# Kernel optimization log

Hardware: AMD Instinct MI355X
Metric: run time of the kernel (lower is better)

Reference implementation:

```python
import jax, jax.numpy as jnp
import numpy as np

N_NODES = 100000

def setup_inputs() -> dict:
    key = jax.random.key(0)
    k1, k2, k3, k4, k5 = jax.random.split(key, 5)
    node_emb = jax.random.normal(k1, (100000, 128), dtype=jnp.float32)
    edge_weight = jax.random.uniform(k2, (1600000,), dtype=jnp.float32)
    src = jax.random.randint(k3, (1600000,), 0, 100000, dtype=jnp.int32)
    dst = jax.random.randint(k4, (1600000,), 0, 100000, dtype=jnp.int32)
    W = jax.random.normal(k5, (128, 128), dtype=jnp.float32) * (1.0 / np.sqrt(128))
    return {"node_emb": node_emb, "edge_weight": edge_weight, "src": src, "dst": dst, "W": W}

def reference(node_emb, edge_weight, src, dst, W):
    # u_mul_e: gather source features, scale by per-edge scalar weight
    msg = node_emb[src] * edge_weight[:, None]          # [E, d]
    # sum reduce into destination nodes (scatter-add / segment-sum)
    agg = jax.ops.segment_sum(msg, dst, num_segments=N_NODES)  # [N, d]
    # linear_out (no bias): agg @ W^T (torch Linear applies x @ W.T)
    return agg @ W.T
```

## Files before the change

### kernel.cpp

```cpp
#include <hip/hip_runtime.h>
#include <cstdint>

typedef unsigned short u16;
typedef unsigned int   u32;

#define DIM     128
#define TPITCH  136
#define BSH     8
#define BSIZE   256
#define NBK_MAX 512
#define CHUNK   4096
#define FBS     128
#define CAP     2560

__device__ __forceinline__ u16 f2bf(float x) {
    u32 u = __float_as_uint(x);
    u32 r = u + 0x7FFFu + ((u >> 16) & 1u);
    return (u16)(r >> 16);
}

typedef __attribute__((ext_vector_type(8))) short bfrag;
typedef __attribute__((ext_vector_type(4))) float f32x4;
typedef __attribute__((ext_vector_type(2))) float f32x2;

__device__ __forceinline__ void transform_role(
    char* smem, const float* __restrict__ A, const float* __restrict__ W,
    u16* __restrict__ Tb, int tile, int n)
{
    u16* Wb = (u16*)smem;
    const int t = threadIdx.x;

    {
        const int j  = t >> 2;
        const int k0 = (t & 3) << 5;
        const float* wr = W + j * DIM + k0;
        u16* wo = Wb + j * TPITCH + k0;
#pragma unroll
        for (int k = 0; k < 32; k += 4) {
            float4 v = *(const float4*)(wr + k);
            ushort4 h;
            h.x = f2bf(v.x); h.y = f2bf(v.y); h.z = f2bf(v.z); h.w = f2bf(v.w);
            *(ushort4*)(wo + k) = h;
        }
    }
    __syncthreads();

    const int wave = t >> 6;
    const int lane = t & 63;
    const int quad = lane >> 4;
    const int l16  = lane & 15;

    const int r0b = tile << 7;
    const int r0  = r0b + (wave << 4);
    const bool active = (r0 < n);

    f32x4 acc[8];
#pragma unroll
    for (int c = 0; c < 8; ++c) acc[c] = (f32x4)(0.f);

    if (active) {
        const int ar = min(r0 + l16, n - 1);
        const float* arow = A + (size_t)ar * DIM;
#pragma unroll
        for (int s = 0; s < 4; ++s) {
            const int koff = (s << 5) + (quad << 3);
            const float4 f0 = *(const float4*)(arow + koff);
            const float4 f1 = *(const float4*)(arow + koff + 4);
            bfrag a;
            a[0] = (short)f2bf(f0.x); a[1] = (short)f2bf(f0.y);
            a[2] = (short)f2bf(f0.z); a[3] = (short)f2bf(f0.w);
            a[4] = (short)f2bf(f1.x); a[5] = (short)f2bf(f1.y);
            a[6] = (short)f2bf(f1.z); a[7] = (short)f2bf(f1.w);
#pragma unroll
            for (int c = 0; c < 8; ++c) {
                const int nn = (c << 4) + l16;
                const bfrag b = *(const bfrag*)(Wb + nn * TPITCH + koff);
                acc[c] = __builtin_amdgcn_mfma_f32_16x16x32_bf16(a, b, acc[c], 0, 0, 0);
            }
        }
    }

    __syncthreads();

    if (active) {
        const int rl0 = (wave << 4) + (quad << 2);
#pragma unroll
        for (int r = 0; r < 4; ++r) {
            u16* trow = Wb + (rl0 + r) * TPITCH + l16;
#pragma unroll
            for (int c = 0; c < 8; ++c)
                trow[c << 4] = f2bf(acc[c][r]);
        }
    }
    __syncthreads();

    {
        const int rl  = t >> 2;
        const int row = r0b + rl;
        if (row < n) {
            const float4* sp = (const float4*)(Wb + rl * TPITCH + ((t & 3) << 5));
            float4* dp = (float4*)(Tb + (size_t)row * DIM + ((t & 3) << 5));
            dp[0] = sp[0];
            dp[1] = sp[1];
            dp[2] = sp[2];
            dp[3] = sp[3];
        }
    }
}

__global__ __launch_bounds__(512) void k_count_transform(
    const int* __restrict__ dst, int* __restrict__ cnt,
    const float* __restrict__ A, const float* __restrict__ W,
    u16* __restrict__ Tb,
    int n, int E, int nCntBlk, int NBK)
{
    __shared__ __align__(16) char smem[49152];
    const int t = threadIdx.x;

    if (blockIdx.x < nCntBlk) {
        int* hist = (int*)smem;
        for (int i = t; i < NBK; i += 512) hist[i] = 0;
        __syncthreads();
        const int base = blockIdx.x * CHUNK;
        const int end  = min(base + CHUNK, E);
        for (int i = base + t; i < end; i += 512)
            atomicAdd(&hist[dst[i] >> BSH], 1);
        __syncthreads();
        for (int b = t; b < NBK; b += 512)
            cnt[b * nCntBlk + blockIdx.x] = hist[b];
        return;
    }

    transform_role(smem, A, W, Tb, blockIdx.x - nCntBlk, n);
}

__global__ __launch_bounds__(256) void k_rowsum(
    const int* __restrict__ cnt, int* __restrict__ tot, int nCntBlk)
{
    __shared__ int red[256];
    const int t = threadIdx.x;
    const int* row = cnt + blockIdx.x * nCntBlk;
    int s = 0;
    for (int i = t; i < nCntBlk; i += 256) s += row[i];
    red[t] = s; __syncthreads();
    for (int o = 128; o; o >>= 1) {
        if (t < o) red[t] += red[t + o];
        __syncthreads();
    }
    if (t == 0) tot[blockIdx.x] = red[0];
}

__global__ __launch_bounds__(512) void k_scan_all(
    const int* __restrict__ tot, int* __restrict__ bucketStart,
    int* __restrict__ cnt, int NBK, int nCntBlk, int E)
{
    __shared__ int sc[512];
    __shared__ int bs;
    const int t = threadIdx.x;
    const int b = blockIdx.x;

    const int v = (t < NBK) ? tot[t] : 0;
    sc[t] = v; __syncthreads();
    for (int d = 1; d < 512; d <<= 1) {
        int u = (t >= d) ? sc[t - d] : 0;
        __syncthreads();
        sc[t] += u;
        __syncthreads();
    }
    if (t == b) bs = sc[t] - v;
    if (b == 0) {
        if (t < NBK) bucketStart[t] = sc[t] - v;
        if (t == 0)  bucketStart[NBK] = E;
    }
    __syncthreads();

    int* row = cnt + b * nCntBlk;
    const int rv = (t < nCntBlk) ? row[t] : 0;
    sc[t] = rv; __syncthreads();
    for (int d = 1; d < 512; d <<= 1) {
        int u = (t >= d) ? sc[t - d] : 0;
        __syncthreads();
        sc[t] += u;
        __syncthreads();
    }
    if (t < nCntBlk) row[t] = bs + sc[t] - rv;
}

__global__ __launch_bounds__(512) void k_scatter_transform(
    const int* __restrict__ src, const int* __restrict__ dst,
    const float* __restrict__ w, const int* __restrict__ cnt,
    const int* __restrict__ bucketStart, int2* __restrict__ es1,
    const float* __restrict__ A, const float* __restrict__ W,
    u16* __restrict__ Tb,
    int n, int E, int nCntBlk, int NBK, int tileOff)
{
    __shared__ __align__(16) char smem[49152];
    const int t = threadIdx.x;

    if (blockIdx.x < nCntBlk) {
        int2* buf   = (int2*)smem;
        u16*  bid   = (u16*)(smem + 32768);
        int*  gbase = (int*)(smem + 40960);
        int*  lbase = (int*)(smem + 43008);
        int*  lpos  = (int*)(smem + 45056);
        int*  sc    = (int*)(smem + 47104);

        const int blk  = blockIdx.x;
        const int base = blk * CHUNK;
        const int end  = min(base + CHUNK, E);
        const int len  = end - base;

        int mylen = 0;
        if (t < NBK) {
            const int g = cnt[t * nCntBlk + blk];
            gbase[t] = g;
            const int nxt = (blk + 1 < nCntBlk) ? cnt[t * nCntBlk + blk + 1]
                                                : bucketStart[t + 1];
            mylen = nxt - g;
        }
        sc[t] = (t < NBK) ? mylen : 0;
        __syncthreads();
        for (int d = 1; d < 512; d <<= 1) {
            int v = (t >= d) ? sc[t - d] : 0;
            __syncthreads();
            sc[t] += v;
            __syncthreads();
        }
        if (t < NBK) {
            const int ex = sc[t] - mylen;
            lbase[t] = ex;
            lpos[t]  = ex;
        }
        __syncthreads();

        for (int i = base + t; i < end; i += 512) {
            const int d   = dst[i];
            const int bkt = d >> BSH;
            const int p   = atomicAdd(&lpos[bkt], 1);
            buf[p] = make_int2(src[i] | ((d & (BSIZE - 1)) << 20),
                               __float_as_int(w[i]));
            bid[p] = (u16)bkt;
        }
        __syncthreads();

        for (int i = t; i < len; i += 512) {
            const int bkt = bid[i];
            es1[gbase[bkt] + (i - lbase[bkt])] = buf[i];
        }
        return;
    }

    transform_role(smem, A, W, Tb, blockIdx.x - nCntBlk + tileOff, n);
}

__global__ __launch_bounds__(512) void gnn_aggregate(
    const u16* __restrict__ Tb, const int* __restrict__ bucketStart,
    const int2* __restrict__ es1, float* __restrict__ out, int n)
{
    __shared__ int2 buf[CAP];
    __shared__ int  cnt[FBS];
    __shared__ int  loff[FBS + 1];
    __shared__ int  cur[FBS];
    __shared__ int  sc[FBS];

    const int f    = blockIdx.x;
    const int c    = f >> 1;
    const int hbit = (f & 1) << 7;
    const int s    = bucketStart[c], e = bucketStart[c + 1];
    const int v0   = f << 7;
    const int t    = threadIdx.x;
    const int lane = t & 63;
    const int wv   = t >> 6;
    const u32* Tw  = (const u32*)Tb;

    if (t < FBS) cnt[t] = 0;
    __syncthreads();
    for (int i = s + t; i < e; i += 512) {
        const int d8 = (es1[i].x >> 20) & 255;
        if ((d8 & 128) == hbit) atomicAdd(&cnt[d8 & 127], 1);
    }
    __syncthreads();

    int myc = 0;
    if (t < FBS) { myc = cnt[t]; sc[t] = myc; }
    __syncthreads();
    for (int d = 1; d < FBS; d <<= 1) {
        int u = 0;
        if (t < FBS && t >= d) u = sc[t - d];
        __syncthreads();
        if (t < FBS) sc[t] += u;
        __syncthreads();
    }
    if (t < FBS) {
        const int ex = sc[t] - myc;
        loff[t] = ex; cur[t] = ex;
        if (t == FBS - 1) loff[FBS] = sc[t];
    }
    __syncthreads();
    const int kept = loff[FBS];

    if (kept <= CAP) {
        for (int i = s + t; i < e; i += 512) {
            const int2 ev = es1[i];
            const int d8 = (ev.x >> 20) & 255;
            if ((d8 & 128) == hbit) {
                const int p = atomicAdd(&cur[d8 & 127], 1);
                buf[p] = make_int2(ev.x & 0xFFFFF, ev.y);
            }
        }
        __syncthreads();

        for (int nt = 0; nt < 16; ++nt) {
            const int tn = (wv << 4) + nt;
            const int v  = v0 + tn;
            if (v >= n) break;
            const int kb = loff[tn], ke = loff[tn + 1];
            float ax0 = 0.f, ay0 = 0.f, ax1 = 0.f, ay1 = 0.f;

            int i = kb;
            for (; i + 7 < ke; i += 8) {
                const int2 e0 = buf[i],     e1 = buf[i + 1], e2 = buf[i + 2], e3 = buf[i + 3];
                const int2 e4 = buf[i + 4], e5 = buf[i + 5], e6 = buf[i + 6], e7 = buf[i + 7];
                const u32 t0 = Tw[(size_t)e0.x * 64 + lane];
                const u32 t1 = Tw[(size_t)e1.x * 64 + lane];
                const u32 t2 = Tw[(size_t)e2.x * 64 + lane];
                const u32 t3 = Tw[(size_t)e3.x * 64 + lane];
                const u32 t4 = Tw[(size_t)e4.x * 64 + lane];
                const u32 t5 = Tw[(size_t)e5.x * 64 + lane];
                const u32 t6 = Tw[(size_t)e6.x * 64 + lane];
                const u32 t7 = Tw[(size_t)e7.x * 64 + lane];
                const float w0 = __int_as_float(e0.y), w1 = __int_as_float(e1.y);
                const float w2 = __int_as_float(e2.y), w3 = __int_as_float(e3.y);
                const float w4 = __int_as_float(e4.y), w5 = __int_as_float(e5.y);
                const float w6 = __int_as_float(e6.y), w7 = __int_as_float(e7.y);
                ax0 += w0 * __uint_as_float(t0 << 16);
                ay0 += w0 * __uint_as_float(t0 & 0xFFFF0000u);
                ax1 += w1 * __uint_as_float(t1 << 16);
                ay1 += w1 * __uint_as_float(t1 & 0xFFFF0000u);
                ax0 += w2 * __uint_as_float(t2 << 16);
                ay0 += w2 * __uint_as_float(t2 & 0xFFFF0000u);
                ax1 += w3 * __uint_as_float(t3 << 16);
                ay1 += w3 * __uint_as_float(t3 & 0xFFFF0000u);
                ax0 += w4 * __uint_as_float(t4 << 16);
                ay0 += w4 * __uint_as_float(t4 & 0xFFFF0000u);
                ax1 += w5 * __uint_as_float(t5 << 16);
                ay1 += w5 * __uint_as_float(t5 & 0xFFFF0000u);
                ax0 += w6 * __uint_as_float(t6 << 16);
                ay0 += w6 * __uint_as_float(t6 & 0xFFFF0000u);
                ax1 += w7 * __uint_as_float(t7 << 16);
                ay1 += w7 * __uint_as_float(t7 & 0xFFFF0000u);
            }
            for (; i + 3 < ke; i += 4) {
                const int2 e0 = buf[i], e1 = buf[i + 1], e2 = buf[i + 2], e3 = buf[i + 3];
                const u32 t0 = Tw[(size_t)e0.x * 64 + lane];
                const u32 t1 = Tw[(size_t)e1.x * 64 + lane];
                const u32 t2 = Tw[(size_t)e2.x * 64 + lane];
                const u32 t3 = Tw[(size_t)e3.x * 64 + lane];
                const float w0 = __int_as_float(e0.y), w1 = __int_as_float(e1.y);
                const float w2 = __int_as_float(e2.y), w3 = __int_as_float(e3.y);
                ax0 += w0 * __uint_as_float(t0 << 16);
                ay0 += w0 * __uint_as_float(t0 & 0xFFFF0000u);
                ax1 += w1 * __uint_as_float(t1 << 16);
                ay1 += w1 * __uint_as_float(t1 & 0xFFFF0000u);
                ax0 += w2 * __uint_as_float(t2 << 16);
                ay0 += w2 * __uint_as_float(t2 & 0xFFFF0000u);
                ax1 += w3 * __uint_as_float(t3 << 16);
                ay1 += w3 * __uint_as_float(t3 & 0xFFFF0000u);
            }
            for (; i < ke; ++i) {
                const int2 ev = buf[i];
                const u32 tv = Tw[(size_t)ev.x * 64 + lane];
                const float w0 = __int_as_float(ev.y);
                ax0 += w0 * __uint_as_float(tv << 16);
                ay0 += w0 * __uint_as_float(tv & 0xFFFF0000u);
            }

            f32x2 r;
            r[0] = ax0 + ax1;
            r[1] = ay0 + ay1;
            __builtin_nontemporal_store(r, (f32x2*)(out + (size_t)v * DIM + 2 * lane));
        }
    } else {
        for (int nt = 0; nt < 16; ++nt) {
            const int tn = (wv << 4) + nt;
            const int v  = v0 + tn;
            if (v >= n) break;
            const int want = hbit | tn;
            float ax = 0.f, ay = 0.f;
            for (int i = s; i < e; ++i) {
                const int2 ev = es1[i];
                if (((ev.x >> 20) & 255) == want) {
                    const u32 tv = Tw[(size_t)(ev.x & 0xFFFFF) * 64 + lane];
                    const float wgt = __int_as_float(ev.y);
                    ax += wgt * __uint_as_float(tv << 16);
                    ay += wgt * __uint_as_float(tv & 0xFFFF0000u);
                }
            }
            f32x2 r; r[0] = ax; r[1] = ay;
            __builtin_nontemporal_store(r, (f32x2*)(out + (size_t)v * DIM + 2 * lane));
        }
    }
}

extern "C" void kernel_launch(void* const* d_in, const int* in_sizes, int n_in,
                              void* d_out, int out_size, void* d_ws, size_t ws_size,
                              hipStream_t stream)
{
    const float* node_emb = (const float*)d_in[0];
    const float* ew       = (const float*)d_in[1];
    const int*   src      = (const int*)d_in[2];
    const int*   dst      = (const int*)d_in[3];
    const float* W        = (const float*)d_in[4];
    float* out = (float*)d_out;

    const int n = in_sizes[0] / DIM;
    const int E = in_sizes[1];
    const int NBK = (n + BSIZE - 1) >> BSH;
    const int nCntBlk = (E + CHUNK - 1) / CHUNK;
    const int M = NBK * nCntBlk;
    const int nfine = (n + FBS - 1) / FBS;

    char* ws = (char*)d_ws;
    size_t o = 0;
    u16* Tb = (u16*)(ws + o);  o += (((size_t)n * DIM * sizeof(u16)) + 255) & ~255ULL;
    int* cnt = (int*)(ws + o); o += (((size_t)M * sizeof(int)) + 255) & ~255ULL;
    int* tot = (int*)(ws + o); o += (((size_t)NBK * sizeof(int)) + 255) & ~255ULL;
    int* bucketStart = (int*)(ws + o); o += (((size_t)(NBK + 1) * sizeof(int)) + 255) & ~255ULL;
    int2* es1 = (int2*)(ws + o);

    const int ntiles = (n + 127) >> 7;
    const int T1 = ntiles >> 1;
    const int T2 = ntiles - T1;

    k_count_transform<<<nCntBlk + T1, 512, 0, stream>>>(
        dst, cnt, node_emb, W, Tb, n, E, nCntBlk, NBK);

    k_rowsum<<<NBK, 256, 0, stream>>>(cnt, tot, nCntBlk);
    k_scan_all<<<NBK, 512, 0, stream>>>(tot, bucketStart, cnt, NBK, nCntBlk, E);

    k_scatter_transform<<<nCntBlk + T2, 512, 0, stream>>>(
        src, dst, ew, cnt, bucketStart, es1, node_emb, W, Tb,
        n, E, nCntBlk, NBK, T1);

    gnn_aggregate<<<nfine, 512, 0, stream>>>(Tb, bucketStart, es1, out, n);
}
```

Measured before the change: 221.8 us.

## Split count kernel from transform and finer-grained histogram chunks

The histogram count kernel no longer co-hosts half of the node-transform tiles; all transform tiles now run alongside the scatter kernel. Counting uses smaller chunks (2048 edges) so more blocks run the short count phase, and the scan is extended to loop over more than 512 columns with a carry. The scatter blocks read every other count column to recover their 4096-edge chunk offsets. This shortens the first kernel but makes the scatter+transform kernel longer, and it doubles the size of the count matrix and the scan work.

```diff
diff --git a/kernel.cpp b/kernel.cpp
--- a/kernel.cpp
+++ b/kernel.cpp
@@ -10,6 +10,7 @@
 #define BSIZE   256
 #define NBK_MAX 512
 #define CHUNK   4096
+#define CHUNKC  2048
 #define FBS     128
 #define CAP     2560
 
@@ -108,40 +109,31 @@
     }
 }
 
-__global__ __launch_bounds__(512) void k_count_transform(
+__global__ __launch_bounds__(512) void k_count(
     const int* __restrict__ dst, int* __restrict__ cnt,
-    const float* __restrict__ A, const float* __restrict__ W,
-    u16* __restrict__ Tb,
-    int n, int E, int nCntBlk, int NBK)
-{
-    __shared__ __align__(16) char smem[49152];
+    int E, int nCB2, int NBK)
+{
+    __shared__ int hist[NBK_MAX];
     const int t = threadIdx.x;
-
-    if (blockIdx.x < nCntBlk) {
-        int* hist = (int*)smem;
-        for (int i = t; i < NBK; i += 512) hist[i] = 0;
-        __syncthreads();
-        const int base = blockIdx.x * CHUNK;
-        const int end  = min(base + CHUNK, E);
-        for (int i = base + t; i < end; i += 512)
-            atomicAdd(&hist[dst[i] >> BSH], 1);
-        __syncthreads();
-        for (int b = t; b < NBK; b += 512)
-            cnt[b * nCntBlk + blockIdx.x] = hist[b];
-        return;
-    }
-
-    transform_role(smem, A, W, Tb, blockIdx.x - nCntBlk, n);
+    for (int i = t; i < NBK; i += 512) hist[i] = 0;
+    __syncthreads();
+    const int base = blockIdx.x * CHUNKC;
+    const int end  = min(base + CHUNKC, E);
+    for (int i = base + t; i < end; i += 512)
+        atomicAdd(&hist[dst[i] >> BSH], 1);
+    __syncthreads();
+    for (int b = t; b < NBK; b += 512)
+        cnt[b * nCB2 + blockIdx.x] = hist[b];
 }
 
 __global__ __launch_bounds__(256) void k_rowsum(
-    const int* __restrict__ cnt, int* __restrict__ tot, int nCntBlk)
+    const int* __restrict__ cnt, int* __restrict__ tot, int nCB2)
 {
     __shared__ int red[256];
     const int t = threadIdx.x;
-    const int* row = cnt + blockIdx.x * nCntBlk;
+    const int* row = cnt + blockIdx.x * nCB2;
     int s = 0;
-    for (int i = t; i < nCntBlk; i += 256) s += row[i];
+    for (int i = t; i < nCB2; i += 256) s += row[i];
     red[t] = s; __syncthreads();
     for (int o = 128; o; o >>= 1) {
         if (t < o) red[t] += red[t + o];
@@ -152,10 +144,11 @@
 
 __global__ __launch_bounds__(512) void k_scan_all(
     const int* __restrict__ tot, int* __restrict__ bucketStart,
-    int* __restrict__ cnt, int NBK, int nCntBlk, int E)
+    int* __restrict__ cnt, int NBK, int nCB2, int E)
 {
     __shared__ int sc[512];
     __shared__ int bs;
+    __shared__ int carry;
     const int t = threadIdx.x;
     const int b = blockIdx.x;
 
@@ -172,18 +165,25 @@
         if (t < NBK) bucketStart[t] = sc[t] - v;
         if (t == 0)  bucketStart[NBK] = E;
     }
-    __syncthreads();
-
-    int* row = cnt + b * nCntBlk;
-    const int rv = (t < nCntBlk) ? row[t] : 0;
-    sc[t] = rv; __syncthreads();
-    for (int d = 1; d < 512; d <<= 1) {
-        int u = (t >= d) ? sc[t - d] : 0;
-        __syncthreads();
-        sc[t] += u;
-        __syncthreads();
-    }
-    if (t < nCntBlk) row[t] = bs + sc[t] - rv;
+    if (t == 0) carry = 0;
+    __syncthreads();
+
+    int* row = cnt + b * nCB2;
+    for (int c0 = 0; c0 < nCB2; c0 += 512) {
+        const int idx = c0 + t;
+        const int rv = (idx < nCB2) ? row[idx] : 0;
+        sc[t] = rv; __syncthreads();
+        for (int d = 1; d < 512; d <<= 1) {
+            int u = (t >= d) ? sc[t - d] : 0;
+            __syncthreads();
+            sc[t] += u;
+            __syncthreads();
+        }
+        if (idx < nCB2) row[idx] = bs + carry + sc[t] - rv;
+        __syncthreads();
+        if (t == 0) carry += sc[511];
+        __syncthreads();
+    }
 }
 
 __global__ __launch_bounds__(512) void k_scatter_transform(
@@ -192,7 +192,7 @@
     const int* __restrict__ bucketStart, int2* __restrict__ es1,
     const float* __restrict__ A, const float* __restrict__ W,
     u16* __restrict__ Tb,
-    int n, int E, int nCntBlk, int NBK, int tileOff)
+    int n, int E, int nCntBlk, int nCB2, int NBK)
 {
     __shared__ __align__(16) char smem[49152];
     const int t = threadIdx.x;
@@ -212,10 +212,11 @@
 
         int mylen = 0;
         if (t < NBK) {
-            const int g = cnt[t * nCntBlk + blk];
+            const int g = cnt[t * nCB2 + 2 * blk];
             gbase[t] = g;
-            const int nxt = (blk + 1 < nCntBlk) ? cnt[t * nCntBlk + blk + 1]
-                                                : bucketStart[t + 1];
+            const int c2 = 2 * blk + 2;
+            const int nxt = (c2 < nCB2) ? cnt[t * nCB2 + c2]
+                                        : bucketStart[t + 1];
             mylen = nxt - g;
         }
         sc[t] = (t < NBK) ? mylen : 0;
@@ -250,7 +251,7 @@
         return;
     }
 
-    transform_role(smem, A, W, Tb, blockIdx.x - nCntBlk + tileOff, n);
+    transform_role(smem, A, W, Tb, blockIdx.x - nCntBlk, n);
 }
 
 __global__ __launch_bounds__(512) void gnn_aggregate(
@@ -417,7 +418,8 @@
     const int E = in_sizes[1];
     const int NBK = (n + BSIZE - 1) >> BSH;
     const int nCntBlk = (E + CHUNK - 1) / CHUNK;
-    const int M = NBK * nCntBlk;
+    const int nCB2 = (E + CHUNKC - 1) / CHUNKC;
+    const int M = NBK * nCB2;
     const int nfine = (n + FBS - 1) / FBS;
 
     char* ws = (char*)d_ws;
@@ -429,18 +431,15 @@
     int2* es1 = (int2*)(ws + o);
 
     const int ntiles = (n + 127) >> 7;
-    const int T1 = ntiles >> 1;
-    const int T2 = ntiles - T1;
-
-    k_count_transform<<<nCntBlk + T1, 512, 0, stream>>>(
-        dst, cnt, node_emb, W, Tb, n, E, nCntBlk, NBK);
-
-    k_rowsum<<<NBK, 256, 0, stream>>>(cnt, tot, nCntBlk);
-    k_scan_all<<<NBK, 512, 0, stream>>>(tot, bucketStart, cnt, NBK, nCntBlk, E);
-
-    k_scatter_transform<<<nCntBlk + T2, 512, 0, stream>>>(
+
+    k_count<<<nCB2, 512, 0, stream>>>(dst, cnt, E, nCB2, NBK);
+
+    k_rowsum<<<NBK, 256, 0, stream>>>(cnt, tot, nCB2);
+    k_scan_all<<<NBK, 512, 0, stream>>>(tot, bucketStart, cnt, NBK, nCB2, E);
+
+    k_scatter_transform<<<nCntBlk + ntiles, 512, 0, stream>>>(
         src, dst, ew, cnt, bucketStart, es1, node_emb, W, Tb,
-        n, E, nCntBlk, NBK, T1);
+        n, E, nCntBlk, nCB2, NBK);
 
     gnn_aggregate<<<nfine, 512, 0, stream>>>(Tb, bucketStart, es1, out, n);
 }
```

Result: no change. 217.8 us (-1.8%).
